# Kernel optimization log

Hardware: AMD Instinct MI355X
Metric: run time of the kernel (lower is better)

Reference implementation:

```python
import jax, jax.numpy as jnp
import numpy as np

B, N, C = 8192, 64, 256  # batch, num_nodes, cells; depth=2


def setup_inputs() -> dict:
    key = jax.random.key(0)
    ks = jax.random.split(key, 9)
    scale1 = 1.0  # fan_in = 1
    scaleC = 1.0 / np.sqrt(C)
    return {
        "Q": jax.random.normal(ks[0], (B, N), dtype=jnp.float32),
        "Y": jax.random.normal(ks[1], (B, N), dtype=jnp.float32),
        # stacked per-node MLP params: Linear(1,C) -> ReLU -> Linear(C,C) -> ReLU -> Linear(C,1)
        "W1": jax.random.normal(ks[2], (N, 1, C), dtype=jnp.float32) * scale1,
        "b1": jax.random.normal(ks[3], (N, C), dtype=jnp.float32) * scale1,
        "W2": jax.random.normal(ks[4], (N, C, C), dtype=jnp.float32) * scaleC,
        "b2": jax.random.normal(ks[5], (N, C), dtype=jnp.float32) * scaleC,
        "W3": jax.random.normal(ks[6], (N, C, 1), dtype=jnp.float32) * scaleC,
        "b3": jax.random.normal(ks[7], (N, 1), dtype=jnp.float32) * scaleC,
        "bias_0": jnp.ones((1, 1), dtype=jnp.float32),
    }


def reference(Q, Y, W1, b1, W2, b2, W3, b3, bias_0):
    s = Q * Y  # [B, N], per-node scalar input s_i = q_i * y_i
    # layer 1: scalar -> C  (W1[n,0,:] broadcast over batch)
    h = jax.nn.relu(s[:, :, None] * W1[None, :, 0, :] + b1[None])  # [B, N, C]
    # layer 2: C -> C, batched over nodes
    h = jax.nn.relu(jnp.einsum("bnc,ncd->bnd", h, W2) + b2[None])  # [B, N, C]
    # layer 3: C -> scalar
    z_i = jnp.einsum("bnc,nc->bn", h, W3[:, :, 0]) + b3[None, :, 0]  # [B, N]
    z_0 = bias_0 - jnp.sum(s, axis=-1, keepdims=True)  # [B, 1]
    z = jnp.concatenate([z_0, z_i], axis=-1)  # [B, N+1]
    z = jax.nn.softmax(z, axis=-1)
    return jax.nn.relu(z)
```

## Files before the change

kernel.cpp:

```cpp
#include <hip/hip_runtime.h>
#include <hip/hip_bf16.h>


typedef unsigned int u32;

__device__ __forceinline__ float row_reduce16(float x) {
    int v;
    v = __builtin_amdgcn_update_dpp(0, __float_as_int(x), 0xB1, 0xF, 0xF, false);
    x += __int_as_float(v);
    v = __builtin_amdgcn_update_dpp(0, __float_as_int(x), 0x4E, 0xF, 0xF, false);
    x += __int_as_float(v);
    v = __builtin_amdgcn_update_dpp(0, __float_as_int(x), 0x124, 0xF, 0xF, false);
    x += __int_as_float(v);
    v = __builtin_amdgcn_update_dpp(0, __float_as_int(x), 0x128, 0xF, 0xF, false);
    x += __int_as_float(v);
    return x;
}

__global__ __launch_bounds__(256) void prep(
    const float* __restrict__ Q, const float* __restrict__ Y,
    const float* __restrict__ W1, const float* __restrict__ b1,
    float* __restrict__ S, float* __restrict__ knots, int* __restrict__ perm)
{
    __shared__ float ts[64][65];
    __shared__ float key[256];
    __shared__ int   idx[256];

    const int blk = blockIdx.x;
    const int tid = threadIdx.x;

    if (blk < 128) {
        const int b0 = blk << 6;
        #pragma unroll
        for (int jj = 0; jj < 16; jj++) {
            int i = tid + (jj << 8);
            int r = i >> 6, c = i & 63;
            ts[r][c] = Q[(size_t)(b0 + r) * 64 + c] * Y[(size_t)(b0 + r) * 64 + c];
        }
        __syncthreads();
        #pragma unroll
        for (int jj = 0; jj < 16; jj++) {
            int i = tid + (jj << 8);
            int nn = i >> 6, bb = i & 63;
            S[((size_t)nn << 13) + b0 + bb] = ts[bb][nn];
        }
    } else {
        const int n = blk - 128;
        {
            float w = W1[n * 256 + tid];
            float b = b1[n * 256 + tid];
            key[tid] = -b / w;
            idx[tid] = tid;
        }
        __syncthreads();
        for (int k = 2; k <= 256; k <<= 1) {
            for (int j = k >> 1; j > 0; j >>= 1) {
                int p = tid ^ j;
                if (p > tid) {
                    float a = key[tid], c = key[p];
                    bool up = ((tid & k) == 0);
                    if (up ? (a > c) : (a < c)) {
                        int ia = idx[tid];
                        key[tid] = c; idx[tid] = idx[p];
                        key[p] = a; idx[p] = ia;
                    }
                }
                __syncthreads();
            }
        }
        knots[n * 256 + tid] = key[tid];
        perm[n * 256 + tid]  = idx[tid];
    }
}

__global__ __launch_bounds__(256) void build_sort(
    const float* __restrict__ W1, const float* __restrict__ b1,
    const float* __restrict__ W2, const float* __restrict__ b2,
    const float* __restrict__ W3, const int* __restrict__ perm,
    const float* __restrict__ S, const float* __restrict__ knots,
    float4* __restrict__ entries, float2* __restrict__ AccP,
    unsigned char* __restrict__ cnt8, uint2* __restrict__ sorted)
{
    __shared__ float w1s[256], b1s[256], kns[256];
    __shared__ int   pm[256];
    __shared__ float part[16][16][8];
    __shared__ u32   hist[257];

    const int blk = blockIdx.x;
    const int tid = threadIdx.x;
    const int lane = tid & 63;

    if (blk < 512) {
        const int n    = blk >> 3;
        const int strip= blk & 7;
        const int prl  = tid & 15;
        const int seg  = tid >> 4;
        const int prg  = (strip << 4) + prl;
        const int d0   = prg << 1;

        w1s[tid] = W1[n * 256 + tid];
        b1s[tid] = b1[n * 256 + tid];
        kns[tid] = knots[n * 256 + tid];
        pm[tid]  = perm[n * 256 + tid];
        __syncthreads();

        const float w30 = W3[n * 256 + d0];
        const float w31 = W3[n * 256 + d0 + 1];
        const float* W2n = W2 + ((size_t)n << 16);
        float2 vreg[16];

        {
            float ba0 = 0.f, bc0 = 0.f, ba1 = 0.f, bc1 = 0.f;
            float da0 = 0.f, dc0 = 0.f, da1 = 0.f, dc1 = 0.f;
            #pragma unroll
            for (int i = 0; i < 16; ++i) {
                int   kj = pm[(seg << 4) + i];
                float w  = w1s[kj];
                float bb = b1s[kj];
                float2 v = *reinterpret_cast<const float2*>(&W2n[kj * 256 + d0]);
                vreg[i] = v;
                if (w < 0.f) {
                    ba0 = fmaf(v.x, w, ba0); bc0 = fmaf(v.x, bb, bc0);
                    ba1 = fmaf(v.y, w, ba1); bc1 = fmaf(v.y, bb, bc1);
                }
                float aw = fabsf(w);
                float cs = (w > 0.f) ? bb : -bb;
                da0 = fmaf(v.x, aw, da0); dc0 = fmaf(v.x, cs, dc0);
                da1 = fmaf(v.y, aw, da1); dc1 = fmaf(v.y, cs, dc1);
            }
            float* p = part[seg][prl];
            p[0] = ba0; p[1] = bc0; p[2] = ba1; p[3] = bc1;
            p[4] = da0; p[5] = dc0; p[6] = da1; p[7] = dc1;
        }
        __syncthreads();

        if (tid < 16) {
            const int pr = tid;
            float sa0 = 0.f, sc0 = 0.f, sa1 = 0.f, sc1 = 0.f;
            #pragma unroll
            for (int sg = 0; sg < 16; ++sg) {
                const float* p = part[sg][pr];
                sa0 += p[0]; sc0 += p[1]; sa1 += p[2]; sc1 += p[3];
            }
            const int dd = ((strip << 4) + pr) << 1;
            sc0 += b2[n * 256 + dd];
            sc1 += b2[n * 256 + dd + 1];

            float k0 = kns[0];
            float hLo0 = (sa0 != 0.f) ? -sa0 : sc0;
            float hHi0 = fmaf(sa0, k0, sc0);
            float hLo1 = (sa1 != 0.f) ? -sa1 : sc1;
            float hHi1 = fmaf(sa1, k0, sc1);
            bool act0 = hLo0 > 0.f && hHi0 > 0.f, drp0 = hLo0 <= 0.f && hHi0 <= 0.f;
            bool act1 = hLo1 > 0.f && hHi1 > 0.f, drp1 = hLo1 <= 0.f && hHi1 <= 0.f;
            bool cr0 = !act0 && !drp0, cr1 = !act1 && !drp1;
            float As = (act0 ? w30 * sa0 : 0.f) + (act1 ? w31 * sa1 : 0.f);
            float Bs = (act0 ? w30 * sc0 : 0.f) + (act1 ? w31 * sc1 : 0.f);
            As = row_reduce16(As); Bs = row_reduce16(Bs);
            u32 cx = (u32)cr0 + (u32)cr1;
            u32 incl = cx, t;
            t = __shfl_up(incl, 1, 64); if (pr >= 1) incl += t;
            t = __shfl_up(incl, 2, 64); if (pr >= 2) incl += t;
            t = __shfl_up(incl, 4, 64); if (pr >= 4) incl += t;
            t = __shfl_up(incl, 8, 64); if (pr >= 8) incl += t;
            u32 excl = incl - cx;
            u32 tot  = __shfl(incl, 15, 64);
            size_t ib = (size_t)(n * 257 + 0) * 8 + strip;
            size_t eb = ib * 32;
            u32 off = excl;
            if (cr0) { entries[eb + off] = make_float4(sa0, sc0, w30, 0.f); off++; }
            if (cr1) { entries[eb + off] = make_float4(sa1, sc1, w31, 0.f); }
            if (pr == 0) {
                AccP[ib] = make_float2(As, Bs);
                cnt8[ib] = (unsigned char)tot;
            }

            float ra0 = sa0, rc0 = sc0, ra1 = sa1, rc1 = sc1;
            #pragma unroll
            for (int sg = 0; sg < 16; ++sg) {
                float* p = part[sg][pr];
                float t4 = p[4], t5 = p[5], t6 = p[6], t7 = p[7];
                p[0] = ra0; p[1] = rc0; p[2] = ra1; p[3] = rc1;
                ra0 += t4; rc0 += t5; ra1 += t6; rc1 += t7;
            }
        }
        __syncthreads();

        {
            const float* p = part[seg][prl];
            float a0 = p[0], c0 = p[1], a1 = p[2], c1 = p[3];
            #pragma unroll 4
            for (int i = 0; i < 16; ++i) {
                int   j  = (seg << 4) + i;
                int   kj = pm[j];
                float w  = w1s[kj];
                float bb = b1s[kj];
                float2 v = vreg[i];
                float aw = fabsf(w);
                float cs = (w > 0.f) ? bb : -bb;
                a0 = fmaf(v.x, aw, a0); c0 = fmaf(v.x, cs, c0);
                a1 = fmaf(v.y, aw, a1); c1 = fmaf(v.y, cs, c1);

                float lo = kns[j];
                float hLo0 = fmaf(a0, lo, c0), hLo1 = fmaf(a1, lo, c1);
                float hHi0, hHi1;
                if (j < 255) {
                    float hi = kns[j + 1];
                    hHi0 = fmaf(a0, hi, c0); hHi1 = fmaf(a1, hi, c1);
                } else {
                    hHi0 = (a0 != 0.f) ? a0 : c0;
                    hHi1 = (a1 != 0.f) ? a1 : c1;
                }
                bool act0 = hLo0 > 0.f && hHi0 > 0.f, drp0 = hLo0 <= 0.f && hHi0 <= 0.f;
                bool act1 = hLo1 > 0.f && hHi1 > 0.f, drp1 = hLo1 <= 0.f && hHi1 <= 0.f;
                bool cr0 = !act0 && !drp0, cr1 = !act1 && !drp1;
                float As = (act0 ? w30 * a0 : 0.f) + (act1 ? w31 * a1 : 0.f);
                float Bs = (act0 ? w30 * c0 : 0.f) + (act1 ? w31 * c1 : 0.f);
                As = row_reduce16(As); Bs = row_reduce16(Bs);
                u32 cx = (u32)cr0 + (u32)cr1;
                u32 incl = cx, t;
                t = __shfl_up(incl, 1, 64); if (prl >= 1) incl += t;
                t = __shfl_up(incl, 2, 64); if (prl >= 2) incl += t;
                t = __shfl_up(incl, 4, 64); if (prl >= 4) incl += t;
                t = __shfl_up(incl, 8, 64); if (prl >= 8) incl += t;
                u32 excl = incl - cx;
                u32 tot  = __shfl(incl, (lane & ~15) + 15, 64);
                size_t ib = (size_t)(n * 257 + (j + 1)) * 8 + strip;
                size_t eb = ib * 32;
                u32 off = excl;
                if (cr0) { entries[eb + off] = make_float4(a0, c0, w30, 0.f); off++; }
                if (cr1) { entries[eb + off] = make_float4(a1, c1, w31, 0.f); }
                if (prl == 0) {
                    AccP[ib] = make_float2(As, Bs);
                    cnt8[ib] = (unsigned char)tot;
                }
            }
        }
    } else {
        const int t = blk - 512;
        const int n = t >> 2;
        const int q = t & 3;

        float* kn = w1s;
        kn[tid] = knots[n * 256 + tid];
        hist[tid] = 0;
        if (tid == 0) hist[256] = 0;
        __syncthreads();

        const float* Sn = S + ((size_t)n << 13) + (q << 11);
        float sv[8]; int iv[8];
        #pragma unroll
        for (int j = 0; j < 8; ++j) {
            const float s = Sn[tid + (j << 8)];
            sv[j] = s;
            int I = 0;
            #pragma unroll
            for (int step = 128; step >= 1; step >>= 1)
                if (kn[I + step - 1] < s) I += step;
            if (I < 256 && kn[I] < s) I += 1;
            iv[j] = I;
            atomicAdd(&hist[I], 1u);
        }
        __syncthreads();

        if (tid < 64) {
            int base = tid << 2;
            u32 h0 = hist[base], h1 = hist[base + 1], h2 = hist[base + 2], h3 = hist[base + 3];
            u32 lsum = h0 + h1 + h2 + h3;
            u32 run = lsum;
            #pragma unroll
            for (int off = 1; off < 64; off <<= 1) {
                u32 tt = __shfl_up(run, off, 64);
                if (lane >= off) run += tt;
            }
            u32 excl = run - lsum;
            hist[base]     = excl;
            hist[base + 1] = excl + h0;
            hist[base + 2] = excl + h0 + h1;
            hist[base + 3] = excl + h0 + h1 + h2;
            if (tid == 63) hist[256] = excl + lsum;
        }
        __syncthreads();

        uint2* dst = sorted + ((size_t)n << 13) + (q << 11);
        #pragma unroll
        for (int j = 0; j < 8; ++j) {
            u32 pos = atomicAdd(&hist[iv[j]], 1u);
            u32 bglob = (u32)((q << 11) + tid + (j << 8));
            dst[pos] = make_uint2(__float_as_uint(sv[j]), ((u32)iv[j] << 13) | bglob);
        }
    }
}

__global__ __launch_bounds__(256) void eval_nodes(
    const uint2* __restrict__ sorted, const float4* __restrict__ entries,
    const float2* __restrict__ AccP, const unsigned char* __restrict__ cnt8,
    const float* __restrict__ b3, float* __restrict__ Z)
{
    const int n   = blockIdx.x;
    const int c0  = blockIdx.y << 8;
    const int tid = threadIdx.x;

    const uint2 ent = sorted[((size_t)n << 13) + c0 + tid];
    const float s   = __uint_as_float(ent.x);
    const int   I   = (int)(ent.y >> 13);
    const int   bl  = (int)(ent.y & 8191u);

    const size_t base = (size_t)(n * 257 + I) * 8;

    float A = 0.f, B = 0.f;
    #pragma unroll
    for (int k = 0; k < 8; ++k) {
        float2 t = AccP[base + k];
        A += t.x; B += t.y;
    }
    float z = fmaf(A, s, B);

    const uint2 cc = *reinterpret_cast<const uint2*>(&cnt8[base]);
    #pragma unroll
    for (int st = 0; st < 8; ++st) {
        u32 c = (st < 4) ? ((cc.x >> (st * 8)) & 0xFFu)
                         : ((cc.y >> ((st - 4) * 8)) & 0xFFu);
        const float4* ep = entries + ((base + st) << 5);
        for (u32 jj = 0; jj < c; ++jj) {
            float4 e = ep[jj];
            z = fmaf(e.z, fmaxf(fmaf(e.x, s, e.y), 0.f), z);
        }
    }
    Z[((size_t)n << 13) + bl] = z + b3[n];
}

__global__ __launch_bounds__(256) void softmax_rows(
    const float* __restrict__ Q, const float* __restrict__ Y,
    const float* __restrict__ Z, const float* __restrict__ bias0,
    float* __restrict__ out)
{
    __shared__ float ts[64][65];
    const int b0   = blockIdx.x << 6;
    const int tid  = threadIdx.x;
    const int lane = tid & 63;
    const int wv   = tid >> 6;

    #pragma unroll
    for (int jj = 0; jj < 16; jj++) {
        int idx = tid + (jj << 8);
        int nn = idx >> 6, bb = idx & 63;
        ts[bb][nn] = Z[((size_t)nn << 13) + b0 + bb];
    }
    __syncthreads();

    const float bias = bias0[0];
    #pragma unroll 2
    for (int r = 0; r < 16; ++r) {
        const int row = (wv << 4) + r;
        const int b   = b0 + row;

        float s = Q[(size_t)b * 64 + lane] * Y[(size_t)b * 64 + lane];
        float ssum = s;
        #pragma unroll
        for (int mask = 32; mask >= 1; mask >>= 1) ssum += __shfl_xor(ssum, mask, 64);
        const float z0 = bias - ssum;

        float zl = ts[row][lane];
        float mx = zl;
        #pragma unroll
        for (int mask = 32; mask >= 1; mask >>= 1) mx = fmaxf(mx, __shfl_xor(mx, mask, 64));
        mx = fmaxf(mx, z0);

        float el = expf(zl - mx);
        float e0 = expf(z0 - mx);
        float den = el;
        #pragma unroll
        for (int mask = 32; mask >= 1; mask >>= 1) den += __shfl_xor(den, mask, 64);
        den += e0;
        const float inv = 1.0f / den;

        out[(size_t)b * 65 + 1 + lane] = el * inv;
        if (lane == 0) out[(size_t)b * 65] = e0 * inv;
    }
}

extern "C" void kernel_launch(void* const* d_in, const int* in_sizes, int n_in,
                              void* d_out, int out_size, void* d_ws, size_t ws_size,
                              hipStream_t stream)
{
    const float* Q     = (const float*)d_in[0];
    const float* Y     = (const float*)d_in[1];
    const float* W1    = (const float*)d_in[2];
    const float* b1    = (const float*)d_in[3];
    const float* W2    = (const float*)d_in[4];
    const float* b2    = (const float*)d_in[5];
    const float* W3    = (const float*)d_in[6];
    const float* b3    = (const float*)d_in[7];
    const float* bias0 = (const float*)d_in[8];
    float* out = (float*)d_out;

    char* ws = (char*)d_ws;
    float4* entries      = (float4*)ws;
    float2* AccP         = (float2*)(ws + 67371008);
    unsigned char* cnt8  = (unsigned char*)(ws + 68423680);
    float* S             = (float*)(ws + 68555264);
    float* Z             = (float*)(ws + 70652416);
    float* knots         = (float*)(ws + 72749568);
    int*   perm          = (int*)  (ws + 72815104);
    uint2* sorted        = (uint2*)(ws + 72880640);

    prep<<<192, 256, 0, stream>>>(Q, Y, W1, b1, S, knots, perm);
    build_sort<<<768, 256, 0, stream>>>(W1, b1, W2, b2, W3, perm, S, knots,
                                        entries, AccP, cnt8, sorted);
    eval_nodes<<<dim3(64, 32), 256, 0, stream>>>(sorted, entries, AccP, cnt8, b3, Z);
    softmax_rows<<<128, 256, 0, stream>>>(Q, Y, Z, bias0, out);
}
```

Before: 55.42 us.

## Compact crossing entries into per-strip streams with prefix-sum offsets

```diff
diff --git a/kernel.cpp b/kernel.cpp
--- a/kernel.cpp
+++ b/kernel.cpp
@@ -3,6 +3,7 @@
 
 
 typedef unsigned int u32;
+#define CAP 8224
 
 __device__ __forceinline__ float row_reduce16(float x) {
     int v;
@@ -79,12 +80,13 @@
     const float* __restrict__ W3, const int* __restrict__ perm,
     const float* __restrict__ S, const float* __restrict__ knots,
     float4* __restrict__ entries, float2* __restrict__ AccP,
-    unsigned char* __restrict__ cnt8, uint2* __restrict__ sorted)
+    unsigned short* __restrict__ offs, uint2* __restrict__ sorted)
 {
-    __shared__ float w1s[256], b1s[256], kns[256];
-    __shared__ int   pm[256];
-    __shared__ float part[16][16][8];
-    __shared__ u32   hist[257];
+    __shared__ float  w1s[256], b1s[256], kns[256];
+    __shared__ int    pm[256];
+    __shared__ float  part[16][16][8];
+    __shared__ float2 accL[257];
+    __shared__ u32    cntU[258];
 
     const int blk = blockIdx.x;
     const int tid = threadIdx.x;
@@ -97,6 +99,7 @@
         const int seg  = tid >> 4;
         const int prg  = (strip << 4) + prl;
         const int d0   = prg << 1;
+        const int g    = (n << 3) + strip;
 
         w1s[tid] = W1[n * 256 + tid];
         b1s[tid] = b1[n * 256 + tid];
@@ -107,6 +110,7 @@
         const float w30 = W3[n * 256 + d0];
         const float w31 = W3[n * 256 + d0 + 1];
         const float* W2n = W2 + ((size_t)n << 16);
+        float4* estream = entries + (size_t)g * CAP;
         float2 vreg[16];
 
         {
@@ -165,15 +169,10 @@
             t = __shfl_up(incl, 8, 64); if (pr >= 8) incl += t;
             u32 excl = incl - cx;
             u32 tot  = __shfl(incl, 15, 64);
-            size_t ib = (size_t)(n * 257 + 0) * 8 + strip;
-            size_t eb = ib * 32;
             u32 off = excl;
-            if (cr0) { entries[eb + off] = make_float4(sa0, sc0, w30, 0.f); off++; }
-            if (cr1) { entries[eb + off] = make_float4(sa1, sc1, w31, 0.f); }
-            if (pr == 0) {
-                AccP[ib] = make_float2(As, Bs);
-                cnt8[ib] = (unsigned char)tot;
-            }
+            if (cr0) { estream[off] = make_float4(sa0, sc0, w30, 0.f); off++; }
+            if (cr1) { estream[off] = make_float4(sa1, sc1, w31, 0.f); }
+            if (pr == 0) { accL[0] = make_float2(As, Bs); cntU[0] = tot; }
 
             float ra0 = sa0, rc0 = sc0, ra1 = sa1, rc1 = sc1;
             #pragma unroll
@@ -223,17 +222,81 @@
                 t = __shfl_up(incl, 2, 64); if (prl >= 2) incl += t;
                 t = __shfl_up(incl, 4, 64); if (prl >= 4) incl += t;
                 t = __shfl_up(incl, 8, 64); if (prl >= 8) incl += t;
+                u32 tot  = __shfl(incl, (lane & ~15) + 15, 64);
+                if (prl == 0) {
+                    accL[j + 1] = make_float2(As, Bs);
+                    cntU[j + 1] = tot;
+                }
+            }
+        }
+        __syncthreads();
+
+        if (tid < 64) {
+            int base = tid << 2;
+            u32 h0 = cntU[base], h1 = cntU[base + 1], h2 = cntU[base + 2], h3 = cntU[base + 3];
+            u32 h4 = (tid == 63) ? cntU[256] : 0u;
+            u32 lsum = h0 + h1 + h2 + h3 + h4;
+            u32 run = lsum;
+            #pragma unroll
+            for (int off = 1; off < 64; off <<= 1) {
+                u32 tt = __shfl_up(run, off, 64);
+                if (lane >= off) run += tt;
+            }
+            u32 excl = run - lsum;
+            cntU[base]     = excl;
+            cntU[base + 1] = excl + h0;
+            cntU[base + 2] = excl + h0 + h1;
+            cntU[base + 3] = excl + h0 + h1 + h2;
+            if (tid == 63) {
+                cntU[256] = excl + h0 + h1 + h2 + h3;
+                cntU[257] = excl + lsum;
+            }
+        }
+        __syncthreads();
+
+        for (int i = tid; i < 257; i += 256)
+            AccP[(size_t)g * 257 + i] = accL[i];
+        for (int i = tid; i < 258; i += 256)
+            offs[(size_t)g * 258 + i] = (unsigned short)cntU[i];
+
+        {
+            const float* p = part[seg][prl];
+            float a0 = p[0], c0 = p[1], a1 = p[2], c1 = p[3];
+            #pragma unroll 4
+            for (int i = 0; i < 16; ++i) {
+                int   j  = (seg << 4) + i;
+                int   kj = pm[j];
+                float w  = w1s[kj];
+                float bb = b1s[kj];
+                float2 v = vreg[i];
+                float aw = fabsf(w);
+                float cs = (w > 0.f) ? bb : -bb;
+                a0 = fmaf(v.x, aw, a0); c0 = fmaf(v.x, cs, c0);
+                a1 = fmaf(v.y, aw, a1); c1 = fmaf(v.y, cs, c1);
+
+                float lo = kns[j];
+                float hLo0 = fmaf(a0, lo, c0), hLo1 = fmaf(a1, lo, c1);
+                float hHi0, hHi1;
+                if (j < 255) {
+                    float hi = kns[j + 1];
+                    hHi0 = fmaf(a0, hi, c0); hHi1 = fmaf(a1, hi, c1);
+                } else {
+                    hHi0 = (a0 != 0.f) ? a0 : c0;
+                    hHi1 = (a1 != 0.f) ? a1 : c1;
+                }
+                bool act0 = hLo0 > 0.f && hHi0 > 0.f, drp0 = hLo0 <= 0.f && hHi0 <= 0.f;
+                bool act1 = hLo1 > 0.f && hHi1 > 0.f, drp1 = hLo1 <= 0.f && hHi1 <= 0.f;
+                bool cr0 = !act0 && !drp0, cr1 = !act1 && !drp1;
+                u32 cx = (u32)cr0 + (u32)cr1;
+                u32 incl = cx, t;
+                t = __shfl_up(incl, 1, 64); if (prl >= 1) incl += t;
+                t = __shfl_up(incl, 2, 64); if (prl >= 2) incl += t;
+                t = __shfl_up(incl, 4, 64); if (prl >= 4) incl += t;
+                t = __shfl_up(incl, 8, 64); if (prl >= 8) incl += t;
                 u32 excl = incl - cx;
-                u32 tot  = __shfl(incl, (lane & ~15) + 15, 64);
-                size_t ib = (size_t)(n * 257 + (j + 1)) * 8 + strip;
-                size_t eb = ib * 32;
-                u32 off = excl;
-                if (cr0) { entries[eb + off] = make_float4(a0, c0, w30, 0.f); off++; }
-                if (cr1) { entries[eb + off] = make_float4(a1, c1, w31, 0.f); }
-                if (prl == 0) {
-                    AccP[ib] = make_float2(As, Bs);
-                    cnt8[ib] = (unsigned char)tot;
-                }
+                u32 off = cntU[j + 1] + excl;
+                if (cr0) { estream[off] = make_float4(a0, c0, w30, 0.f); off++; }
+                if (cr1) { estream[off] = make_float4(a1, c1, w31, 0.f); }
             }
         }
     } else {
@@ -242,6 +305,7 @@
         const int q = t & 3;
 
         float* kn = w1s;
+        u32* hist = cntU;
         kn[tid] = knots[n * 256 + tid];
         hist[tid] = 0;
         if (tid == 0) hist[256] = 0;
@@ -294,7 +358,7 @@
 
 __global__ __launch_bounds__(256) void eval_nodes(
     const uint2* __restrict__ sorted, const float4* __restrict__ entries,
-    const float2* __restrict__ AccP, const unsigned char* __restrict__ cnt8,
+    const float2* __restrict__ AccP, const unsigned short* __restrict__ offs,
     const float* __restrict__ b3, float* __restrict__ Z)
 {
     const int n   = blockIdx.x;
@@ -306,28 +370,21 @@
     const int   I   = (int)(ent.y >> 13);
     const int   bl  = (int)(ent.y & 8191u);
 
-    const size_t base = (size_t)(n * 257 + I) * 8;
-
-    float A = 0.f, B = 0.f;
-    #pragma unroll
-    for (int k = 0; k < 8; ++k) {
-        float2 t = AccP[base + k];
-        A += t.x; B += t.y;
-    }
-    float z = fmaf(A, s, B);
-
-    const uint2 cc = *reinterpret_cast<const uint2*>(&cnt8[base]);
+    float A = 0.f, B = 0.f, zc = 0.f;
     #pragma unroll
     for (int st = 0; st < 8; ++st) {
-        u32 c = (st < 4) ? ((cc.x >> (st * 8)) & 0xFFu)
-                         : ((cc.y >> ((st - 4) * 8)) & 0xFFu);
-        const float4* ep = entries + ((base + st) << 5);
-        for (u32 jj = 0; jj < c; ++jj) {
+        const int g = (n << 3) + st;
+        float2 ap = AccP[(size_t)g * 257 + I];
+        A += ap.x; B += ap.y;
+        const unsigned short* op = offs + (size_t)g * 258 + I;
+        u32 o0 = op[0], o1 = op[1];
+        const float4* ep = entries + (size_t)g * CAP;
+        for (u32 jj = o0; jj < o1; ++jj) {
             float4 e = ep[jj];
-            z = fmaf(e.z, fmaxf(fmaf(e.x, s, e.y), 0.f), z);
+            zc = fmaf(e.z, fmaxf(fmaf(e.x, s, e.y), 0.f), zc);
         }
     }
-    Z[((size_t)n << 13) + bl] = z + b3[n];
+    Z[((size_t)n << 13) + bl] = fmaf(A, s, B) + zc + b3[n];
 }
 
 __global__ __launch_bounds__(256) void softmax_rows(
@@ -396,18 +453,18 @@
     float* out = (float*)d_out;
 
     char* ws = (char*)d_ws;
-    float4* entries      = (float4*)ws;
-    float2* AccP         = (float2*)(ws + 67371008);
-    unsigned char* cnt8  = (unsigned char*)(ws + 68423680);
-    float* S             = (float*)(ws + 68555264);
-    float* Z             = (float*)(ws + 70652416);
-    float* knots         = (float*)(ws + 72749568);
-    int*   perm          = (int*)  (ws + 72815104);
-    uint2* sorted        = (uint2*)(ws + 72880640);
+    float4* entries       = (float4*)ws;
+    float2* AccP          = (float2*)(ws + 67371008);
+    unsigned short* offs  = (unsigned short*)(ws + 68423680);
+    float* S              = (float*)(ws + 68687872);
+    float* Z              = (float*)(ws + 70785024);
+    float* knots          = (float*)(ws + 72882176);
+    int*   perm           = (int*)  (ws + 72947712);
+    uint2* sorted         = (uint2*)(ws + 73013248);
 
     prep<<<192, 256, 0, stream>>>(Q, Y, W1, b1, S, knots, perm);
     build_sort<<<768, 256, 0, stream>>>(W1, b1, W2, b2, W3, perm, S, knots,
-                                        entries, AccP, cnt8, sorted);
-    eval_nodes<<<dim3(64, 32), 256, 0, stream>>>(sorted, entries, AccP, cnt8, b3, Z);
+                                        entries, AccP, offs, sorted);
+    eval_nodes<<<dim3(64, 32), 256, 0, stream>>>(sorted, entries, AccP, offs, b3, Z);
     softmax_rows<<<128, 256, 0, stream>>>(Q, Y, Z, bias0, out);
 }
```

Result: slower. 62.40 us (+12.6%).
